# Kernel tuning notes

Hardware: AMD Instinct MI355X
Metric: run time of the kernel (lower is better)

## Reference

```python
import jax, jax.numpy as jnp
import numpy as np

N = 100000   # num nodes / num_embs
D = 64       # dim
E = 1200000  # num edges (before self-loops)
L = 2        # num_layers
H = 1        # heads
EPS = 1e-5
NEG_SLOPE = 0.2


def setup_inputs() -> dict:
    key = jax.random.key(0)
    ks = jax.random.split(key, 12)
    return {
        "x": jax.random.normal(ks[0], (N, D), jnp.float32),  # unused by forward (matches torch)
        "edge_index": jax.random.randint(ks[1], (2, E), 0, N, dtype=jnp.int64),
        "emb_weight": jax.random.normal(ks[2], (N, D), jnp.float32) * 0.1,
        "ln_gamma": jnp.ones((L, D), jnp.float32),
        "ln_beta": jnp.zeros((L, D), jnp.float32),
        "Wl": jax.random.normal(ks[3], (L, D, H * D), jnp.float32) * 0.05,
        "Wr": jax.random.normal(ks[4], (L, D, H * D), jnp.float32) * 0.05,
        "att": jax.random.normal(ks[5], (L, H, D), jnp.float32) * 0.05,
        "conv_bias": jnp.zeros((L, D), jnp.float32),
        "post_w": jax.random.normal(ks[6], (D, D), jnp.float32) * 0.05,
        "post_b": jnp.zeros((D,), jnp.float32),
    }


def _layernorm(x, g, b):
    # pyg LayerNorm(mode='node'): per-node normalization over features
    mu = jnp.mean(x, axis=-1, keepdims=True)
    var = jnp.var(x, axis=-1, keepdims=True)
    return (x - mu) * jax.lax.rsqrt(var + EPS) * g + b


def _gatv2(x, src, tgt, Wl, Wr, a, bias):
    # x: [N, D]; Wl/Wr: [D, H*D]; a: [H, D]
    xl = (x @ Wl).reshape(N, H, D)  # source transform
    xr = (x @ Wr).reshape(N, H, D)  # target transform
    m = jax.nn.leaky_relu(xl[src] + xr[tgt], NEG_SLOPE)      # [Et, H, D]
    e = jnp.einsum('ehd,hd->eh', m, a)                       # [Et, H]
    # segment softmax over edges grouped by target node
    emax = jax.ops.segment_max(e, tgt, num_segments=N)       # [N, H]
    ex = jnp.exp(e - emax[tgt])
    denom = jax.ops.segment_sum(ex, tgt, num_segments=N)
    alpha = ex / (denom[tgt] + 1e-16)                        # [Et, H]
    out = jax.ops.segment_sum(xl[src] * alpha[..., None], tgt, num_segments=N)  # [N, H, D]
    return out.mean(axis=1) + bias                           # concat=False -> mean over heads


def reference(x, edge_index, emb_weight, ln_gamma, ln_beta, Wl, Wr, att, conv_bias, post_w, post_b):
    # GATv2Conv default add_self_loops=True
    loops = jnp.arange(N, dtype=edge_index.dtype)
    src = jnp.concatenate([edge_index[0], loops])
    tgt = jnp.concatenate([edge_index[1], loops])
    h = emb_weight  # forward replaces input x with embedding table
    for i in range(L):
        y = _layernorm(h, ln_gamma[i], ln_beta[i])
        y = _gatv2(y, src, tgt, Wl[i], Wr[i], att[i], conv_bias[i])
        y = jax.nn.gelu(y, approximate=False)
        h = y + h  # residual
    return h @ post_w + post_b
```

## Files before the change

### kernel.cpp

```cpp
#include <hip/hip_runtime.h>
#include <math.h>

#define NN 100000
#define DD 64
#define NE 1200000
#define NB 391
#define SCH 2048
#define BCAP 4096
#define CCAP (BCAP + 256)
#define GB ((NN + 63) / 64)
#define HS 88

typedef __attribute__((ext_vector_type(8))) short bf16x8;
typedef __attribute__((ext_vector_type(4))) float f32x4;
typedef __attribute__((ext_vector_type(2))) float f32x2;

#if __has_builtin(__builtin_amdgcn_exp2f)
#define EXP2(x) __builtin_amdgcn_exp2f(x)
#else
#define EXP2(x) exp2f(x)
#endif

__device__ __forceinline__ unsigned short f2bf(float x) {
    unsigned u = __float_as_uint(x);
    return (unsigned short)((u + 0x7FFFu + ((u >> 16) & 1u)) >> 16);
}
__device__ __forceinline__ float bf2f(unsigned short b) {
    return __uint_as_float(((unsigned)b) << 16);
}

__device__ __forceinline__ float gelu_exact(float x) {
    return 0.5f * x * (1.0f + erff(x * 0.70710678118654752f));
}

__device__ __forceinline__ float row16_sum(float x) {
    int t;
    t = __builtin_amdgcn_update_dpp(0, __float_as_int(x), 0x121, 0xf, 0xf, true);
    x += __int_as_float(t);
    t = __builtin_amdgcn_update_dpp(0, __float_as_int(x), 0x122, 0xf, 0xf, true);
    x += __int_as_float(t);
    t = __builtin_amdgcn_update_dpp(0, __float_as_int(x), 0x124, 0xf, 0xf, true);
    x += __int_as_float(t);
    t = __builtin_amdgcn_update_dpp(0, __float_as_int(x), 0x128, 0xf, 0xf, true);
    x += __int_as_float(t);
    return x;
}

__global__ __launch_bounds__(128) void k_wall(
    const float* __restrict__ Wl, const float* __restrict__ Wr,
    const float* __restrict__ g, const float* __restrict__ be,
    const float* __restrict__ pw, const float* __restrict__ pb,
    unsigned short* __restrict__ aT0, unsigned short* __restrict__ aT1,
    unsigned short* __restrict__ fT,
    float* __restrict__ S0, float* __restrict__ C0,
    float* __restrict__ S1, float* __restrict__ C1, float* __restrict__ Cf,
    int* __restrict__ bkcur)
{
    const int blk = blockIdx.x;
    const int c = threadIdx.x;
    if (blk < 2) {
        const float* WL = Wl + blk * DD * DD;
        const float* WR = Wr + blk * DD * DD;
        const float* gg = g + blk * DD;
        const float* bb = be + blk * DD;
        unsigned short* aT = blk ? aT1 : aT0;
        float* S = blk ? S1 : S0;
        float* C = blk ? C1 : C0;
        const float* W = (c < 64) ? WL : WR;
        const int cc = c & 63;
        float s = 0.f, cC = 0.f;
        unsigned short* hi_p = aT + c * 64;
        unsigned short* lo_p = aT + 128 * 64 + c * 64;
        #pragma unroll 8
        for (int k = 0; k < 64; ++k) {
            float w = W[k * 64 + cc];
            float a = gg[k] * w;
            unsigned short hi = f2bf(a);
            unsigned short lo = f2bf(a - bf2f(hi));
            hi_p[k] = hi; lo_p[k] = lo;
            s += a;
            cC = fmaf(bb[k], w, cC);
        }
        S[c] = s; C[c] = cC;
    } else {
        if (c < 64) {
            unsigned short* hi_p = fT + c * 64;
            unsigned short* lo_p = fT + 64 * 64 + c * 64;
            #pragma unroll 8
            for (int k = 0; k < 64; ++k) {
                float w = pw[k * 64 + c];
                unsigned short hi = f2bf(w);
                unsigned short lo = f2bf(w - bf2f(hi));
                hi_p[k] = hi; lo_p[k] = lo;
            }
            Cf[c] = pb[c];
        } else {
            for (int i = c - 64; i < NB; i += 64) bkcur[i] = i * BCAP;
        }
    }
}

__global__ __launch_bounds__(256) void k_bscatter(const int* __restrict__ src, const int* __restrict__ tgt,
                                                  int* __restrict__ bkcur, unsigned int* __restrict__ ebuf) {
    __shared__ int stgt[SCH];
    __shared__ unsigned short srk[SCH];
    __shared__ int hist[NB];
    __shared__ int hbase[NB];
    const int base = blockIdx.x * SCH;
    const int cnt = min(SCH, NE - base);
    const int tid = threadIdx.x;
    for (int i = tid; i < NB; i += 256) hist[i] = 0;
    for (int i = tid; i < cnt; i += 256) stgt[i] = tgt[base + i];
    __syncthreads();
    for (int i = tid; i < cnt; i += 256)
        srk[i] = (unsigned short)atomicAdd(&hist[stgt[i] >> 8], 1);
    __syncthreads();
    for (int b = tid; b < NB; b += 256) {
        int c = hist[b];
        hbase[b] = c ? atomicAdd(&bkcur[b], c) : 0;
    }
    __syncthreads();
    for (int i = tid; i < cnt; i += 256) {
        int t = stgt[i];
        unsigned int e = ((unsigned int)src[base + i] << 8) | (unsigned int)(t & 255);
        ebuf[hbase[t >> 8] + (int)srk[i]] = e;
    }
}

template<int CTW, bool LN>
__device__ __forceinline__ void gemm_tile(
    const int tile, unsigned short* hbh, unsigned short* hbl,
    float* smean, float* srho,
    const float* __restrict__ h, const unsigned short* __restrict__ aT,
    const float* __restrict__ S, const float* __restrict__ C,
    unsigned short* __restrict__ xlb, unsigned short* __restrict__ xrb,
    float* __restrict__ outp)
{
    const int tid = threadIdx.x;
    {
        const int row = tid >> 2, q = tid & 3;
        const int node = min(tile + row, NN - 1);
        const float* hp = h + (size_t)node * DD + q * 16;
        float4 v[4];
        #pragma unroll
        for (int i = 0; i < 4; ++i) v[i] = *(const float4*)(hp + i * 4);
        if (LN) {
            float sum = 0.f, ssq = 0.f;
            #pragma unroll
            for (int i = 0; i < 4; ++i) {
                sum += v[i].x + v[i].y + v[i].z + v[i].w;
                ssq += v[i].x * v[i].x + v[i].y * v[i].y + v[i].z * v[i].z + v[i].w * v[i].w;
            }
            sum += __shfl_xor(sum, 1, 64); ssq += __shfl_xor(ssq, 1, 64);
            sum += __shfl_xor(sum, 2, 64); ssq += __shfl_xor(ssq, 2, 64);
            if (q == 0) {
                float mean = sum * 0.015625f;
                float var = ssq * 0.015625f - mean * mean;
                smean[row] = mean;
                srho[row] = rsqrtf(var + 1e-5f);
            }
        }
        #pragma unroll
        for (int half = 0; half < 2; ++half) {
            bf16x8 ph, pl;
            #pragma unroll
            for (int e = 0; e < 8; ++e) {
                float f = (&v[half * 2 + (e >> 2)].x)[e & 3];
                unsigned short hi = f2bf(f);
                unsigned short lo = f2bf(f - bf2f(hi));
                ph[e] = (short)hi; pl[e] = (short)lo;
            }
            const int so = row * HS + q * 16 + half * 8;
            *(bf16x8*)&hbh[so] = ph;
            *(bf16x8*)&hbl[so] = pl;
        }
    }
    __syncthreads();
    const int lane = tid & 63;
    const int wslot = tid >> 6;
    const int li16 = lane & 15;
    const int g16 = lane >> 4;
    const int NCT = CTW * 4;
    f32x4 acc[CTW][4];
    #pragma unroll
    for (int c = 0; c < CTW; ++c)
        #pragma unroll
        for (int rt = 0; rt < 4; ++rt) acc[c][rt] = (f32x4){0.f, 0.f, 0.f, 0.f};
    #pragma unroll
    for (int kk = 0; kk < 2; ++kk) {
        bf16x8 ah[4], al[4];
        #pragma unroll
        for (int rt = 0; rt < 4; ++rt) {
            const int so = (rt * 16 + li16) * HS + kk * 32 + g16 * 8;
            ah[rt] = *(const bf16x8*)&hbh[so];
            al[rt] = *(const bf16x8*)&hbl[so];
        }
        #pragma unroll
        for (int c = 0; c < CTW; ++c) {
            const int ct = wslot + c * 4;
            const unsigned short* bp = aT + (ct * 16 + li16) * 64 + kk * 32 + g16 * 8;
            bf16x8 bh = *(const bf16x8*)bp;
            bf16x8 bl = *(const bf16x8*)(bp + NCT * 16 * 64);
            #pragma unroll
            for (int rt = 0; rt < 4; ++rt) {
                acc[c][rt] = __builtin_amdgcn_mfma_f32_16x16x32_bf16(ah[rt], bh, acc[c][rt], 0, 0, 0);
                acc[c][rt] = __builtin_amdgcn_mfma_f32_16x16x32_bf16(al[rt], bh, acc[c][rt], 0, 0, 0);
                acc[c][rt] = __builtin_amdgcn_mfma_f32_16x16x32_bf16(ah[rt], bl, acc[c][rt], 0, 0, 0);
            }
        }
    }
    #pragma unroll
    for (int c = 0; c < CTW; ++c) {
        const int ct = wslot + c * 4;
        const int col = ct * 16 + li16;
        const float Cc = C[col];
        float Sc = 0.f;
        if (LN) Sc = S[col];
        #pragma unroll
        for (int rt = 0; rt < 4; ++rt) {
            const int r0 = rt * 16 + g16 * 4;
            #pragma unroll
            for (int j = 0; j < 4; ++j) {
                const int row2 = r0 + j;
                const int node = tile + row2;
                if (node < NN) {
                    float p = acc[c][rt][j];
                    if (LN) {
                        float val = fmaf(srho[row2], p - smean[row2] * Sc, Cc);
                        unsigned short* xb = (ct < 4) ? xlb : xrb;
                        xb[(size_t)node * DD + (col & 63)] = f2bf(val);
                    } else {
                        outp[(size_t)node * DD + col] = p + Cc;
                    }
                }
            }
        }
    }
}

template<int CTW, bool LN>
__global__ __launch_bounds__(256) void k_gemm(
    const float* __restrict__ h, const unsigned short* __restrict__ aT,
    const float* __restrict__ S, const float* __restrict__ C,
    unsigned short* __restrict__ xlb, unsigned short* __restrict__ xrb,
    float* __restrict__ outp)
{
    __shared__ __align__(16) unsigned short hbh[64 * HS];
    __shared__ __align__(16) unsigned short hbl[64 * HS];
    __shared__ float smean[64], srho[64];
    gemm_tile<CTW, LN>(blockIdx.x * 64, hbh, hbl, smean, srho,
                       h, aT, S, C, xlb, xrb, outp);
}

__global__ __launch_bounds__(256) void k_bfg(
    const int* __restrict__ bkcur, const unsigned int* __restrict__ ebuf,
    int2* __restrict__ rowse, int* __restrict__ csr,
    const float* __restrict__ h, const unsigned short* __restrict__ aT,
    const float* __restrict__ S, const float* __restrict__ C,
    unsigned short* __restrict__ xlb, unsigned short* __restrict__ xrb)
{
    __shared__ __align__(16) unsigned short hbh[64 * HS];
    __shared__ __align__(16) unsigned short hbl[64 * HS];
    __shared__ float smean[64], srho[64];
    __shared__ int hist[256];
    __shared__ int pos[256];
    __shared__ int wsum[4];
    if (blockIdx.x < NB) {
        const int b = blockIdx.x, tid = threadIdx.x;
        const int bb = b * BCAP;
        const int be = bkcur[b];
        hist[tid] = 0;
        __syncthreads();
        for (int i = bb + tid; i < be; i += 256) atomicAdd(&hist[ebuf[i] & 255u], 1);
        __syncthreads();
        const int v = hist[tid];
        const int lane = tid & 63, w = tid >> 6;
        int sc = v;
        #pragma unroll
        for (int o = 1; o < 64; o <<= 1) { int t = __shfl_up(sc, o, 64); if (lane >= o) sc += t; }
        if (lane == 63) wsum[w] = sc;
        __syncthreads();
        int off = 0;
        for (int k = 0; k < w; ++k) off += wsum[k];
        const int node = b * 256 + tid;
        const int rp = b * CCAP + off + sc - v + tid;
        if (node < NN) {
            rowse[node] = make_int2(rp, rp + 1 + v);
            csr[rp] = node << 6;
        }
        pos[tid] = rp + 1;
        __syncthreads();
        for (int i = bb + tid; i < be; i += 256) {
            unsigned int e = ebuf[i];
            int p = atomicAdd(&pos[e & 255u], 1);
            csr[p] = (int)(e >> 8) << 6;
        }
    } else {
        gemm_tile<2, true>((blockIdx.x - NB) * 64, hbh, hbl, smean, srho,
                           h, aT, S, C, xlb, xrb, nullptr);
    }
}

__global__ __launch_bounds__(256) void k_agg(
    const int2* __restrict__ rowse, const int* __restrict__ csr,
    const unsigned short* __restrict__ xlb, const unsigned short* __restrict__ xrb,
    const float* __restrict__ att, const float* __restrict__ cbias,
    const float* __restrict__ h_in, float* __restrict__ h_out)
{
    const int lane = threadIdx.x & 63;
    const int li   = lane & 15;
    const int sub  = lane >> 4;
    const int li4  = li * 4;
    const int fidx = li4 + sub;
    const int wid  = (blockIdx.x * 256 + threadIdx.x) >> 6;
    const int nw   = gridDim.x * 4;
    const float L2E = 1.4426950408889634f;
    const float4 ar = *(const float4*)&att[li4];
    const f32x2 a1_01  = {L2E * ar.x, L2E * ar.y};
    const f32x2 a1_23  = {L2E * ar.z, L2E * ar.w};
    const f32x2 a02_01 = {0.2f * L2E * ar.x, 0.2f * L2E * ar.y};
    const f32x2 a02_23 = {0.2f * L2E * ar.z, 0.2f * L2E * ar.w};
    const float cb = cbias[fidx];
    const f32x2 z2 = {0.f, 0.f};
    for (int n = wid; n < NN; n += nw) {
        const uint2 xru = *(const uint2*)&xrb[(size_t)n * DD + li4];
        f32x2 xrt01, xrt23;
        xrt01.x = __uint_as_float(xru.x << 16);
        xrt01.y = __uint_as_float(xru.x & 0xFFFF0000u);
        xrt23.x = __uint_as_float(xru.y << 16);
        xrt23.y = __uint_as_float(xru.y & 0xFFFF0000u);
        const int2 se = rowse[n];
        const int beg = se.x, end = se.y;
        const int end1 = end - 1;
        int j0 = beg + sub;
        int j1 = j0 + 4;
        int j2 = j0 + 8;
        uint2 v0 = *(const uint2*)&xlb[(unsigned)csr[min(j0, end1)] + li4];
        uint2 v1 = *(const uint2*)&xlb[(unsigned)csr[min(j1, end1)] + li4];
        uint2 v2 = *(const uint2*)&xlb[(unsigned)csr[min(j2, end1)] + li4];
        float den = 0.f;
        f32x2 acc01 = z2, acc23 = z2;
        const int nch = (end - beg + 3) >> 2;
        for (int c = 0; c < nch; ++c) {
            const uint2 cur = v0;
            const int jcur = j0;
            v0 = v1; v1 = v2;
            j0 = j1; j1 = j2; j2 += 4;
            v2 = *(const uint2*)&xlb[(unsigned)csr[min(j2, end1)] + li4];
            f32x2 f01, f23;
            f01.x = __uint_as_float(cur.x << 16);
            f01.y = __uint_as_float(cur.x & 0xFFFF0000u);
            f23.x = __uint_as_float(cur.y << 16);
            f23.y = __uint_as_float(cur.y & 0xFFFF0000u);
            const f32x2 t01 = f01 + xrt01;
            const f32x2 t23 = f23 + xrt23;
            f32x2 pv = __builtin_elementwise_max(t01, z2) * a1_01;
            pv = __builtin_elementwise_min(t01, z2) * a02_01 + pv;
            pv = __builtin_elementwise_max(t23, z2) * a1_23 + pv;
            pv = __builtin_elementwise_min(t23, z2) * a02_23 + pv;
            float p = row16_sum(pv.x + pv.y);
            float ex = (jcur < end) ? EXP2(p) : 0.f;
            den += ex;
            const f32x2 ex2 = {ex, ex};
            acc01 = f01 * ex2 + acc01;
            acc23 = f23 * ex2 + acc23;
        }
        #pragma unroll
        for (int o = 16; o < 64; o <<= 1) {
            acc01.x += __shfl_xor(acc01.x, o, 64);
            acc01.y += __shfl_xor(acc01.y, o, 64);
            acc23.x += __shfl_xor(acc23.x, o, 64);
            acc23.y += __shfl_xor(acc23.y, o, 64);
            den     += __shfl_xor(den,     o, 64);
        }
        const float id = 1.f / (den + 1e-16f);
        const float v01 = (sub & 1) ? acc01.y : acc01.x;
        const float v23 = (sub & 1) ? acc23.y : acc23.x;
        const float val = (sub & 2) ? v23 : v01;
        const float o = gelu_exact(fmaf(val, id, cb)) + h_in[(size_t)n * DD + fidx];
        h_out[(size_t)n * DD + fidx] = o;
    }
}

extern "C" void kernel_launch(void* const* d_in, const int* in_sizes, int n_in,
                              void* d_out, int out_size, void* d_ws, size_t ws_size,
                              hipStream_t stream) {
    const int*   edge_index = (const int*)d_in[1];
    const int*   src   = edge_index;
    const int*   tgt   = edge_index + NE;
    const float* emb   = (const float*)d_in[2];
    const float* ln_g  = (const float*)d_in[3];
    const float* ln_b  = (const float*)d_in[4];
    const float* Wl    = (const float*)d_in[5];
    const float* Wr    = (const float*)d_in[6];
    const float* att   = (const float*)d_in[7];
    const float* cbias = (const float*)d_in[8];
    const float* pw    = (const float*)d_in[9];
    const float* pb    = (const float*)d_in[10];
    float* out = (float*)d_out;

    unsigned short* xlb = (unsigned short*)d_ws;
    unsigned short* xrb = xlb + (size_t)NN * DD;
    int* csr            = (int*)(xrb + (size_t)NN * DD);
    unsigned int* ebuf  = (unsigned int*)(csr + NB * CCAP);
    int2* rowse         = (int2*)(ebuf + (size_t)NB * BCAP);
    int* bkcur          = (int*)(rowse + NN);
    unsigned short* aT0 = (unsigned short*)(bkcur + 400);
    unsigned short* aT1 = aT0 + 2 * 128 * 64;
    unsigned short* fT  = aT1 + 2 * 128 * 64;
    float* S0 = (float*)(fT + 2 * 64 * 64);
    float* C0 = S0 + 128;
    float* S1 = C0 + 128;
    float* C1 = S1 + 128;
    float* Cf = C1 + 128;

    const int AGG_BLOCKS = 2048;

    k_wall<<<3, 128, 0, stream>>>(Wl, Wr, ln_g, ln_b, pw, pb,
                                  aT0, aT1, fT, S0, C0, S1, C1, Cf, bkcur);

    k_bscatter<<<(NE + SCH - 1) / SCH, 256, 0, stream>>>(src, tgt, bkcur, ebuf);

    k_bfg<<<NB + GB, 256, 0, stream>>>(bkcur, ebuf, rowse, csr,
                                       emb, aT0, S0, C0, xlb, xrb);

    k_agg<<<AGG_BLOCKS, 256, 0, stream>>>(rowse, csr, xlb, xrb, att, cbias, emb, out);

    k_gemm<2, true><<<GB, 256, 0, stream>>>(out, aT1, S1, C1, xlb, xrb, nullptr);

    k_agg<<<AGG_BLOCKS, 256, 0, stream>>>(rowse, csr, xlb, xrb, att + DD, cbias + DD, out, out);

    k_gemm<1, false><<<GB, 256, 0, stream>>>(out, fT, nullptr, Cf, nullptr, nullptr, out);
}
```

Baseline: 218.2 us.

## Fuse weight prep into bucket scatter and interleave two nodes per wave in aggregation

```diff
diff --git a/kernel.cpp b/kernel.cpp
--- a/kernel.cpp
+++ b/kernel.cpp
@@ -6,6 +6,7 @@
 #define NE 1200000
 #define NB 391
 #define SCH 2048
+#define SCB ((NE + SCH - 1) / SCH)
 #define BCAP 4096
 #define CCAP (BCAP + 256)
 #define GB ((NN + 63) / 64)
@@ -46,19 +47,19 @@
     return x;
 }
 
-__global__ __launch_bounds__(128) void k_wall(
+__device__ __forceinline__ void wall_body(
+    int blk, int tid,
     const float* __restrict__ Wl, const float* __restrict__ Wr,
     const float* __restrict__ g, const float* __restrict__ be,
     const float* __restrict__ pw, const float* __restrict__ pb,
     unsigned short* __restrict__ aT0, unsigned short* __restrict__ aT1,
     unsigned short* __restrict__ fT,
     float* __restrict__ S0, float* __restrict__ C0,
-    float* __restrict__ S1, float* __restrict__ C1, float* __restrict__ Cf,
-    int* __restrict__ bkcur)
-{
-    const int blk = blockIdx.x;
-    const int c = threadIdx.x;
+    float* __restrict__ S1, float* __restrict__ C1, float* __restrict__ Cf)
+{
     if (blk < 2) {
+        if (tid >= 128) return;
+        const int c = tid;
         const float* WL = Wl + blk * DD * DD;
         const float* WR = Wr + blk * DD * DD;
         const float* gg = g + blk * DD;
@@ -83,29 +84,41 @@
         }
         S[c] = s; C[c] = cC;
     } else {
-        if (c < 64) {
-            unsigned short* hi_p = fT + c * 64;
-            unsigned short* lo_p = fT + 64 * 64 + c * 64;
-            #pragma unroll 8
-            for (int k = 0; k < 64; ++k) {
-                float w = pw[k * 64 + c];
-                unsigned short hi = f2bf(w);
-                unsigned short lo = f2bf(w - bf2f(hi));
-                hi_p[k] = hi; lo_p[k] = lo;
-            }
-            Cf[c] = pb[c];
-        } else {
-            for (int i = c - 64; i < NB; i += 64) bkcur[i] = i * BCAP;
-        }
-    }
-}
-
-__global__ __launch_bounds__(256) void k_bscatter(const int* __restrict__ src, const int* __restrict__ tgt,
-                                                  int* __restrict__ bkcur, unsigned int* __restrict__ ebuf) {
+        if (tid >= 64) return;
+        const int c = tid;
+        unsigned short* hi_p = fT + c * 64;
+        unsigned short* lo_p = fT + 64 * 64 + c * 64;
+        #pragma unroll 8
+        for (int k = 0; k < 64; ++k) {
+            float w = pw[k * 64 + c];
+            unsigned short hi = f2bf(w);
+            unsigned short lo = f2bf(w - bf2f(hi));
+            hi_p[k] = hi; lo_p[k] = lo;
+        }
+        Cf[c] = pb[c];
+    }
+}
+
+__global__ __launch_bounds__(256) void k_bsw(
+    const int* __restrict__ src, const int* __restrict__ tgt,
+    int* __restrict__ bkcnt, unsigned int* __restrict__ ebuf,
+    const float* __restrict__ Wl, const float* __restrict__ Wr,
+    const float* __restrict__ g, const float* __restrict__ be,
+    const float* __restrict__ pw, const float* __restrict__ pb,
+    unsigned short* __restrict__ aT0, unsigned short* __restrict__ aT1,
+    unsigned short* __restrict__ fT,
+    float* __restrict__ S0, float* __restrict__ C0,
+    float* __restrict__ S1, float* __restrict__ C1, float* __restrict__ Cf)
+{
     __shared__ int stgt[SCH];
     __shared__ unsigned short srk[SCH];
     __shared__ int hist[NB];
     __shared__ int hbase[NB];
+    if (blockIdx.x >= SCB) {
+        wall_body(blockIdx.x - SCB, threadIdx.x, Wl, Wr, g, be, pw, pb,
+                  aT0, aT1, fT, S0, C0, S1, C1, Cf);
+        return;
+    }
     const int base = blockIdx.x * SCH;
     const int cnt = min(SCH, NE - base);
     const int tid = threadIdx.x;
@@ -117,7 +130,7 @@
     __syncthreads();
     for (int b = tid; b < NB; b += 256) {
         int c = hist[b];
-        hbase[b] = c ? atomicAdd(&bkcur[b], c) : 0;
+        hbase[b] = c ? (b * BCAP + atomicAdd(&bkcnt[b], c)) : 0;
     }
     __syncthreads();
     for (int i = tid; i < cnt; i += 256) {
@@ -253,7 +266,7 @@
 }
 
 __global__ __launch_bounds__(256) void k_bfg(
-    const int* __restrict__ bkcur, const unsigned int* __restrict__ ebuf,
+    const int* __restrict__ bkcnt, const unsigned int* __restrict__ ebuf,
     int2* __restrict__ rowse, int* __restrict__ csr,
     const float* __restrict__ h, const unsigned short* __restrict__ aT,
     const float* __restrict__ S, const float* __restrict__ C,
@@ -268,7 +281,7 @@
     if (blockIdx.x < NB) {
         const int b = blockIdx.x, tid = threadIdx.x;
         const int bb = b * BCAP;
-        const int be = bkcur[b];
+        const int be = bb + bkcnt[b];
         hist[tid] = 0;
         __syncthreads();
         for (int i = bb + tid; i < be; i += 256) atomicAdd(&hist[ebuf[i] & 255u], 1);
@@ -313,7 +326,7 @@
     const int li4  = li * 4;
     const int fidx = li4 + sub;
     const int wid  = (blockIdx.x * 256 + threadIdx.x) >> 6;
-    const int nw   = gridDim.x * 4;
+    const int W    = gridDim.x * 4;
     const float L2E = 1.4426950408889634f;
     const float4 ar = *(const float4*)&att[li4];
     const f32x2 a1_01  = {L2E * ar.x, L2E * ar.y};
@@ -322,64 +335,95 @@
     const f32x2 a02_23 = {0.2f * L2E * ar.z, 0.2f * L2E * ar.w};
     const float cb = cbias[fidx];
     const f32x2 z2 = {0.f, 0.f};
-    for (int n = wid; n < NN; n += nw) {
-        const uint2 xru = *(const uint2*)&xrb[(size_t)n * DD + li4];
-        f32x2 xrt01, xrt23;
-        xrt01.x = __uint_as_float(xru.x << 16);
-        xrt01.y = __uint_as_float(xru.x & 0xFFFF0000u);
-        xrt23.x = __uint_as_float(xru.y << 16);
-        xrt23.y = __uint_as_float(xru.y & 0xFFFF0000u);
-        const int2 se = rowse[n];
-        const int beg = se.x, end = se.y;
-        const int end1 = end - 1;
-        int j0 = beg + sub;
-        int j1 = j0 + 4;
-        int j2 = j0 + 8;
-        uint2 v0 = *(const uint2*)&xlb[(unsigned)csr[min(j0, end1)] + li4];
-        uint2 v1 = *(const uint2*)&xlb[(unsigned)csr[min(j1, end1)] + li4];
-        uint2 v2 = *(const uint2*)&xlb[(unsigned)csr[min(j2, end1)] + li4];
-        float den = 0.f;
-        f32x2 acc01 = z2, acc23 = z2;
-        const int nch = (end - beg + 3) >> 2;
-        for (int c = 0; c < nch; ++c) {
-            const uint2 cur = v0;
-            const int jcur = j0;
-            v0 = v1; v1 = v2;
-            j0 = j1; j1 = j2; j2 += 4;
-            v2 = *(const uint2*)&xlb[(unsigned)csr[min(j2, end1)] + li4];
-            f32x2 f01, f23;
-            f01.x = __uint_as_float(cur.x << 16);
-            f01.y = __uint_as_float(cur.x & 0xFFFF0000u);
-            f23.x = __uint_as_float(cur.y << 16);
-            f23.y = __uint_as_float(cur.y & 0xFFFF0000u);
-            const f32x2 t01 = f01 + xrt01;
-            const f32x2 t23 = f23 + xrt23;
-            f32x2 pv = __builtin_elementwise_max(t01, z2) * a1_01;
-            pv = __builtin_elementwise_min(t01, z2) * a02_01 + pv;
-            pv = __builtin_elementwise_max(t23, z2) * a1_23 + pv;
-            pv = __builtin_elementwise_min(t23, z2) * a02_23 + pv;
-            float p = row16_sum(pv.x + pv.y);
-            float ex = (jcur < end) ? EXP2(p) : 0.f;
-            den += ex;
-            const f32x2 ex2 = {ex, ex};
-            acc01 = f01 * ex2 + acc01;
-            acc23 = f23 * ex2 + acc23;
+
+#define LOAD_XR(nS, xr01S, xr23S) { \
+    const uint2 xru = *(const uint2*)&xrb[(size_t)(nS) * DD + li4]; \
+    xr01S.x = __uint_as_float(xru.x << 16); \
+    xr01S.y = __uint_as_float(xru.x & 0xFFFF0000u); \
+    xr23S.x = __uint_as_float(xru.y << 16); \
+    xr23S.y = __uint_as_float(xru.y & 0xFFFF0000u); }
+
+#define CHUNK_STEP(j0S, j1S, v0S, v1S, endS, end1S, denS, acc01S, acc23S, xr01S, xr23S) { \
+    const uint2 cur = v0S; const int jc = j0S; \
+    v0S = v1S; j0S = j1S; j1S += 4; \
+    if (j1S <= end1S) v1S = *(const uint2*)&xlb[(unsigned)csr[j1S] + li4]; \
+    f32x2 f01, f23; \
+    f01.x = __uint_as_float(cur.x << 16); \
+    f01.y = __uint_as_float(cur.x & 0xFFFF0000u); \
+    f23.x = __uint_as_float(cur.y << 16); \
+    f23.y = __uint_as_float(cur.y & 0xFFFF0000u); \
+    const f32x2 t01 = f01 + xr01S; \
+    const f32x2 t23 = f23 + xr23S; \
+    f32x2 pv = __builtin_elementwise_max(t01, z2) * a1_01; \
+    pv = __builtin_elementwise_min(t01, z2) * a02_01 + pv; \
+    pv = __builtin_elementwise_max(t23, z2) * a1_23 + pv; \
+    pv = __builtin_elementwise_min(t23, z2) * a02_23 + pv; \
+    float p = row16_sum(pv.x + pv.y); \
+    float ex = (jc < endS) ? EXP2(p) : 0.f; \
+    denS += ex; \
+    const f32x2 ex2 = {ex, ex}; \
+    acc01S = f01 * ex2 + acc01S; \
+    acc23S = f23 * ex2 + acc23S; }
+
+    for (int nA = wid; nA < NN; nA += 2 * W) {
+        const int nB = nA + W;
+        const bool vB = nB < NN;
+        f32x2 xr01A, xr23A, xr01B, xr23B;
+        LOAD_XR(nA, xr01A, xr23A);
+        LOAD_XR(vB ? nB : nA, xr01B, xr23B);
+        const int2 seA = rowse[nA];
+        const int2 seB = rowse[vB ? nB : nA];
+        const int begA = seA.x, endA = seA.y;
+        const int begB = seB.x, endB = vB ? seB.y : seB.x;
+        const int end1A = endA - 1, end1B = endB - 1;
+        int j0A = begA + sub, j1A = j0A + 4;
+        int j0B = begB + sub, j1B = j0B + 4;
+        uint2 v0A = {0u, 0u}, v1A = {0u, 0u}, v0B = {0u, 0u}, v1B = {0u, 0u};
+        if (j0A <= end1A) v0A = *(const uint2*)&xlb[(unsigned)csr[j0A] + li4];
+        if (j0B <= end1B) v0B = *(const uint2*)&xlb[(unsigned)csr[j0B] + li4];
+        if (j1A <= end1A) v1A = *(const uint2*)&xlb[(unsigned)csr[j1A] + li4];
+        if (j1B <= end1B) v1B = *(const uint2*)&xlb[(unsigned)csr[j1B] + li4];
+        float denA = 0.f, denB = 0.f;
+        f32x2 acc01A = z2, acc23A = z2, acc01B = z2, acc23B = z2;
+        const int nchA = (endA - begA + 3) >> 2;
+        const int nchB = (endB - begB + 3) >> 2;
+        const int nchM = max(nchA, nchB);
+        for (int c = 0; c < nchM; ++c) {
+            CHUNK_STEP(j0A, j1A, v0A, v1A, endA, end1A, denA, acc01A, acc23A, xr01A, xr23A);
+            CHUNK_STEP(j0B, j1B, v0B, v1B, endB, end1B, denB, acc01B, acc23B, xr01B, xr23B);
         }
         #pragma unroll
         for (int o = 16; o < 64; o <<= 1) {
-            acc01.x += __shfl_xor(acc01.x, o, 64);
-            acc01.y += __shfl_xor(acc01.y, o, 64);
-            acc23.x += __shfl_xor(acc23.x, o, 64);
-            acc23.y += __shfl_xor(acc23.y, o, 64);
-            den     += __shfl_xor(den,     o, 64);
-        }
-        const float id = 1.f / (den + 1e-16f);
-        const float v01 = (sub & 1) ? acc01.y : acc01.x;
-        const float v23 = (sub & 1) ? acc23.y : acc23.x;
-        const float val = (sub & 2) ? v23 : v01;
-        const float o = gelu_exact(fmaf(val, id, cb)) + h_in[(size_t)n * DD + fidx];
-        h_out[(size_t)n * DD + fidx] = o;
-    }
+            acc01A.x += __shfl_xor(acc01A.x, o, 64);
+            acc01A.y += __shfl_xor(acc01A.y, o, 64);
+            acc23A.x += __shfl_xor(acc23A.x, o, 64);
+            acc23A.y += __shfl_xor(acc23A.y, o, 64);
+            denA     += __shfl_xor(denA,     o, 64);
+            acc01B.x += __shfl_xor(acc01B.x, o, 64);
+            acc01B.y += __shfl_xor(acc01B.y, o, 64);
+            acc23B.x += __shfl_xor(acc23B.x, o, 64);
+            acc23B.y += __shfl_xor(acc23B.y, o, 64);
+            denB     += __shfl_xor(denB,     o, 64);
+        }
+        {
+            const float id = 1.f / (denA + 1e-16f);
+            const float w01 = (sub & 1) ? acc01A.y : acc01A.x;
+            const float w23 = (sub & 1) ? acc23A.y : acc23A.x;
+            const float val = (sub & 2) ? w23 : w01;
+            const float o = gelu_exact(fmaf(val, id, cb)) + h_in[(size_t)nA * DD + fidx];
+            h_out[(size_t)nA * DD + fidx] = o;
+        }
+        if (vB) {
+            const float id = 1.f / (denB + 1e-16f);
+            const float w01 = (sub & 1) ? acc01B.y : acc01B.x;
+            const float w23 = (sub & 1) ? acc23B.y : acc23B.x;
+            const float val = (sub & 2) ? w23 : w01;
+            const float o = gelu_exact(fmaf(val, id, cb)) + h_in[(size_t)nB * DD + fidx];
+            h_out[(size_t)nB * DD + fidx] = o;
+        }
+    }
+#undef CHUNK_STEP
+#undef LOAD_XR
 }
 
 extern "C" void kernel_launch(void* const* d_in, const int* in_sizes, int n_in,
@@ -404,8 +448,8 @@
     int* csr            = (int*)(xrb + (size_t)NN * DD);
     unsigned int* ebuf  = (unsigned int*)(csr + NB * CCAP);
     int2* rowse         = (int2*)(ebuf + (size_t)NB * BCAP);
-    int* bkcur          = (int*)(rowse + NN);
-    unsigned short* aT0 = (unsigned short*)(bkcur + 400);
+    int* bkcnt          = (int*)(rowse + NN);
+    unsigned short* aT0 = (unsigned short*)(bkcnt + 400);
     unsigned short* aT1 = aT0 + 2 * 128 * 64;
     unsigned short* fT  = aT1 + 2 * 128 * 64;
     float* S0 = (float*)(fT + 2 * 64 * 64);
@@ -416,12 +460,13 @@
 
     const int AGG_BLOCKS = 2048;
 
-    k_wall<<<3, 128, 0, stream>>>(Wl, Wr, ln_g, ln_b, pw, pb,
-                                  aT0, aT1, fT, S0, C0, S1, C1, Cf, bkcur);
-
-    k_bscatter<<<(NE + SCH - 1) / SCH, 256, 0, stream>>>(src, tgt, bkcur, ebuf);
-
-    k_bfg<<<NB + GB, 256, 0, stream>>>(bkcur, ebuf, rowse, csr,
+    hipMemsetAsync(bkcnt, 0, NB * sizeof(int), stream);
+
+    k_bsw<<<SCB + 3, 256, 0, stream>>>(src, tgt, bkcnt, ebuf,
+                                       Wl, Wr, ln_g, ln_b, pw, pb,
+                                       aT0, aT1, fT, S0, C0, S1, C1, Cf);
+
+    k_bfg<<<NB + GB, 256, 0, stream>>>(bkcnt, ebuf, rowse, csr,
                                        emb, aT0, S0, C0, xlb, xrb);
 
     k_agg<<<AGG_BLOCKS, 256, 0, stream>>>(rowse, csr, xlb, xrb, att, cbias, emb, out);
```

Result: slower. 250.7 us (+14.9%).

## Fuse weight-prep into bucket-scatter kernel and shorten gather prefetch depth

Applied to the files above, without the earlier changes.

```diff
diff --git a/kernel.cpp b/kernel.cpp
--- a/kernel.cpp
+++ b/kernel.cpp
@@ -6,6 +6,7 @@
 #define NE 1200000
 #define NB 391
 #define SCH 2048
+#define SCB ((NE + SCH - 1) / SCH)
 #define BCAP 4096
 #define CCAP (BCAP + 256)
 #define GB ((NN + 63) / 64)
@@ -46,19 +47,19 @@
     return x;
 }
 
-__global__ __launch_bounds__(128) void k_wall(
+__device__ __forceinline__ void wall_body(
+    int blk, int tid,
     const float* __restrict__ Wl, const float* __restrict__ Wr,
     const float* __restrict__ g, const float* __restrict__ be,
     const float* __restrict__ pw, const float* __restrict__ pb,
     unsigned short* __restrict__ aT0, unsigned short* __restrict__ aT1,
     unsigned short* __restrict__ fT,
     float* __restrict__ S0, float* __restrict__ C0,
-    float* __restrict__ S1, float* __restrict__ C1, float* __restrict__ Cf,
-    int* __restrict__ bkcur)
-{
-    const int blk = blockIdx.x;
-    const int c = threadIdx.x;
+    float* __restrict__ S1, float* __restrict__ C1, float* __restrict__ Cf)
+{
     if (blk < 2) {
+        if (tid >= 128) return;
+        const int c = tid;
         const float* WL = Wl + blk * DD * DD;
         const float* WR = Wr + blk * DD * DD;
         const float* gg = g + blk * DD;
@@ -83,29 +84,41 @@
         }
         S[c] = s; C[c] = cC;
     } else {
-        if (c < 64) {
-            unsigned short* hi_p = fT + c * 64;
-            unsigned short* lo_p = fT + 64 * 64 + c * 64;
-            #pragma unroll 8
-            for (int k = 0; k < 64; ++k) {
-                float w = pw[k * 64 + c];
-                unsigned short hi = f2bf(w);
-                unsigned short lo = f2bf(w - bf2f(hi));
-                hi_p[k] = hi; lo_p[k] = lo;
-            }
-            Cf[c] = pb[c];
-        } else {
-            for (int i = c - 64; i < NB; i += 64) bkcur[i] = i * BCAP;
-        }
-    }
-}
-
-__global__ __launch_bounds__(256) void k_bscatter(const int* __restrict__ src, const int* __restrict__ tgt,
-                                                  int* __restrict__ bkcur, unsigned int* __restrict__ ebuf) {
+        if (tid >= 64) return;
+        const int c = tid;
+        unsigned short* hi_p = fT + c * 64;
+        unsigned short* lo_p = fT + 64 * 64 + c * 64;
+        #pragma unroll 8
+        for (int k = 0; k < 64; ++k) {
+            float w = pw[k * 64 + c];
+            unsigned short hi = f2bf(w);
+            unsigned short lo = f2bf(w - bf2f(hi));
+            hi_p[k] = hi; lo_p[k] = lo;
+        }
+        Cf[c] = pb[c];
+    }
+}
+
+__global__ __launch_bounds__(256) void k_bsw(
+    const int* __restrict__ src, const int* __restrict__ tgt,
+    int* __restrict__ bkcnt, unsigned int* __restrict__ ebuf,
+    const float* __restrict__ Wl, const float* __restrict__ Wr,
+    const float* __restrict__ g, const float* __restrict__ be,
+    const float* __restrict__ pw, const float* __restrict__ pb,
+    unsigned short* __restrict__ aT0, unsigned short* __restrict__ aT1,
+    unsigned short* __restrict__ fT,
+    float* __restrict__ S0, float* __restrict__ C0,
+    float* __restrict__ S1, float* __restrict__ C1, float* __restrict__ Cf)
+{
     __shared__ int stgt[SCH];
     __shared__ unsigned short srk[SCH];
     __shared__ int hist[NB];
     __shared__ int hbase[NB];
+    if (blockIdx.x >= SCB) {
+        wall_body(blockIdx.x - SCB, threadIdx.x, Wl, Wr, g, be, pw, pb,
+                  aT0, aT1, fT, S0, C0, S1, C1, Cf);
+        return;
+    }
     const int base = blockIdx.x * SCH;
     const int cnt = min(SCH, NE - base);
     const int tid = threadIdx.x;
@@ -117,7 +130,7 @@
     __syncthreads();
     for (int b = tid; b < NB; b += 256) {
         int c = hist[b];
-        hbase[b] = c ? atomicAdd(&bkcur[b], c) : 0;
+        hbase[b] = c ? (b * BCAP + atomicAdd(&bkcnt[b], c)) : 0;
     }
     __syncthreads();
     for (int i = tid; i < cnt; i += 256) {
@@ -253,7 +266,7 @@
 }
 
 __global__ __launch_bounds__(256) void k_bfg(
-    const int* __restrict__ bkcur, const unsigned int* __restrict__ ebuf,
+    const int* __restrict__ bkcnt, const unsigned int* __restrict__ ebuf,
     int2* __restrict__ rowse, int* __restrict__ csr,
     const float* __restrict__ h, const unsigned short* __restrict__ aT,
     const float* __restrict__ S, const float* __restrict__ C,
@@ -268,7 +281,7 @@
     if (blockIdx.x < NB) {
         const int b = blockIdx.x, tid = threadIdx.x;
         const int bb = b * BCAP;
-        const int be = bkcur[b];
+        const int be = bb + bkcnt[b];
         hist[tid] = 0;
         __syncthreads();
         for (int i = bb + tid; i < be; i += 256) atomicAdd(&hist[ebuf[i] & 255u], 1);
@@ -332,21 +345,20 @@
         const int2 se = rowse[n];
         const int beg = se.x, end = se.y;
         const int end1 = end - 1;
-        int j0 = beg + sub;
-        int j1 = j0 + 4;
-        int j2 = j0 + 8;
-        uint2 v0 = *(const uint2*)&xlb[(unsigned)csr[min(j0, end1)] + li4];
-        uint2 v1 = *(const uint2*)&xlb[(unsigned)csr[min(j1, end1)] + li4];
-        uint2 v2 = *(const uint2*)&xlb[(unsigned)csr[min(j2, end1)] + li4];
+        int j  = beg + sub;
+        int jn = j + 4;
+        uint2 v  = *(const uint2*)&xlb[(unsigned)csr[min(j,  end1)] + li4];
+        uint2 vn = *(const uint2*)&xlb[(unsigned)csr[min(jn, end1)] + li4];
         float den = 0.f;
         f32x2 acc01 = z2, acc23 = z2;
         const int nch = (end - beg + 3) >> 2;
         for (int c = 0; c < nch; ++c) {
-            const uint2 cur = v0;
-            const int jcur = j0;
-            v0 = v1; v1 = v2;
-            j0 = j1; j1 = j2; j2 += 4;
-            v2 = *(const uint2*)&xlb[(unsigned)csr[min(j2, end1)] + li4];
+            const uint2 cur = v;
+            const int jcur = j;
+            v = vn;
+            j = jn;
+            jn += 4;
+            vn = *(const uint2*)&xlb[(unsigned)csr[min(jn, end1)] + li4];
             f32x2 f01, f23;
             f01.x = __uint_as_float(cur.x << 16);
             f01.y = __uint_as_float(cur.x & 0xFFFF0000u);
@@ -404,8 +416,8 @@
     int* csr            = (int*)(xrb + (size_t)NN * DD);
     unsigned int* ebuf  = (unsigned int*)(csr + NB * CCAP);
     int2* rowse         = (int2*)(ebuf + (size_t)NB * BCAP);
-    int* bkcur          = (int*)(rowse + NN);
-    unsigned short* aT0 = (unsigned short*)(bkcur + 400);
+    int* bkcnt          = (int*)(rowse + NN);
+    unsigned short* aT0 = (unsigned short*)(bkcnt + 400);
     unsigned short* aT1 = aT0 + 2 * 128 * 64;
     unsigned short* fT  = aT1 + 2 * 128 * 64;
     float* S0 = (float*)(fT + 2 * 64 * 64);
@@ -416,12 +428,13 @@
 
     const int AGG_BLOCKS = 2048;
 
-    k_wall<<<3, 128, 0, stream>>>(Wl, Wr, ln_g, ln_b, pw, pb,
-                                  aT0, aT1, fT, S0, C0, S1, C1, Cf, bkcur);
-
-    k_bscatter<<<(NE + SCH - 1) / SCH, 256, 0, stream>>>(src, tgt, bkcur, ebuf);
-
-    k_bfg<<<NB + GB, 256, 0, stream>>>(bkcur, ebuf, rowse, csr,
+    hipMemsetAsync(bkcnt, 0, NB * sizeof(int), stream);
+
+    k_bsw<<<SCB + 3, 256, 0, stream>>>(src, tgt, bkcnt, ebuf,
+                                       Wl, Wr, ln_g, ln_b, pw, pb,
+                                       aT0, aT1, fT, S0, C0, S1, C1, Cf);
+
+    k_bfg<<<NB + GB, 256, 0, stream>>>(bkcnt, ebuf, rowse, csr,
                                        emb, aT0, S0, C0, xlb, xrb);
 
     k_agg<<<AGG_BLOCKS, 256, 0, stream>>>(rowse, csr, xlb, xrb, att, cbias, emb, out);
```

After: 220.5 us. No clear change (+1.1%).
